# Kernel optimization log

Hardware: AMD Instinct MI355X
Metric: run time of the kernel (lower is better)

The kernel has to match this reference:

```python
import jax, jax.numpy as jnp
import numpy as np

B, C_IN, C_OUT, H, W_SP = 64, 256, 256, 32, 32
G = H * W_SP  # groups == H*W per module assert


def setup_inputs() -> dict:
    key = jax.random.key(0)
    k1, k2, k3 = jax.random.split(key, 3)
    x = jax.random.normal(k1, (B, C_IN, H, W_SP), dtype=jnp.float32)
    # grouped 1x1 conv == per-group linear: weight [G, C_out, C_in], bias [G, C_out]
    W = jax.random.normal(k2, (G, C_OUT, C_IN), dtype=jnp.float32) * (1.0 / np.sqrt(C_IN))
    b = jax.random.normal(k3, (G, C_OUT), dtype=jnp.float32) * 0.01
    return {"x": x, "W": W, "b": b}


def reference(x, W, b):
    Bn, Cin, Hn, Wn = x.shape
    Gn = Hn * Wn
    # permute(0,2,3,1).reshape(B,-1,1,1): channels-last flatten -> [B, G, C_in]
    xg = jnp.transpose(x, (0, 2, 3, 1)).reshape(Bn, Gn, Cin)
    # block-diagonal batched matmul per spatial position (group)
    out = jnp.einsum("bgi,goi->bgo", xg, W) + b  # [B, G, C_out]
    # view(B,H,W,C_out).permute(0,3,1,2)
    return jnp.transpose(out.reshape(Bn, Hn, Wn, -1), (0, 3, 1, 2))
```

## Files before the change

kernel.cpp:

```cpp
#include <hip/hip_runtime.h>
#include <hip/hip_bf16.h>

typedef __bf16 bf16x8 __attribute__((ext_vector_type(8)));
typedef float f32x4 __attribute__((ext_vector_type(4)));

#define GN    1024
#define BATCH 64
#define CIN   256
#define COUT  256
#define NG    4
#define A_ELEMS (BATCH * CIN)
#define WSLICE  8192

#define G_AS __attribute__((address_space(1)))
#define L_AS __attribute__((address_space(3)))

static __device__ __forceinline__ void gload16(const void* g, void* l) {
  __builtin_amdgcn_global_load_lds((const G_AS void*)g, (L_AS void*)l, 16, 0, 0);
}

static __device__ __forceinline__ ushort f2bf(float f) {
  __hip_bfloat16 h = __float2bfloat16(f);
  return *reinterpret_cast<ushort*>(&h);
}
static __device__ __forceinline__ float bf2f(ushort u) {
  uint v = (uint)u << 16;
  return *reinterpret_cast<float*>(&v);
}

__global__ __launch_bounds__(256) void k_transpose_convert(
    const float* __restrict__ x, ushort* __restrict__ xT)
{
  __shared__ float tile[64][65];
  const int g0 = blockIdx.x * 64;
  const int i0 = blockIdx.y * 64;
  const int b  = blockIdx.z;
  const int t  = threadIdx.x;
  const int a  = t & 15;
  const int r  = t >> 4;
  const int key = (b & 7) << 3;

  const float* xb = x + (size_t)b * CIN * GN;
#pragma unroll
  for (int p = 0; p < 4; ++p) {
    int ii = p * 16 + r;
    float4 v = *reinterpret_cast<const float4*>(
        &xb[(size_t)(i0 + ii) * GN + g0 + a * 4]);
    tile[ii][a * 4 + 0] = v.x;
    tile[ii][a * 4 + 1] = v.y;
    tile[ii][a * 4 + 2] = v.z;
    tile[ii][a * 4 + 3] = v.w;
  }
  __syncthreads();

  ushort* xTb = xT + (size_t)b * GN * CIN;
#pragma unroll
  for (int p = 0; p < 4; ++p) {
    int gg = p * 16 + r;
    ushort4 u;
    u.x = f2bf(tile[a * 4 + 0][gg]);
    u.y = f2bf(tile[a * 4 + 1][gg]);
    u.z = f2bf(tile[a * 4 + 2][gg]);
    u.w = f2bf(tile[a * 4 + 3][gg]);
    int isw = (i0 + a * 4) ^ key;
    *reinterpret_cast<ushort4*>(&xTb[(size_t)(g0 + gg) * CIN + isw]) = u;
  }
}

__global__ __launch_bounds__(256) void k_group_gemm(
    const ushort* __restrict__ xT, const float* __restrict__ W,
    const float* __restrict__ bias, float* __restrict__ out,
    ushort* __restrict__ outT, int use_ws)
{
  __shared__ __align__(16) unsigned char lds[2 * A_ELEMS * 2 + 4 * 2 * WSLICE];
  ushort* lA        = (ushort*)lds;
  unsigned char* lW = lds + 2 * A_ELEMS * 2;

  const int tid  = threadIdx.x;
  const int wave = tid >> 6;
  const int lane = tid & 63;
  const int g_base = blockIdx.x * NG;

  const int arow = lane & 15;
  const int colk = (lane >> 4) * 32;
  const int kq   = (lane >> 4) << 3;
  const int oc   = 64 * wave + arow;

  unsigned char* lWw = lW + wave * (2 * WSLICE);
  const int swz_src = ((lane & 7) ^ (lane >> 3)) << 4;
  const int wrow    = lane >> 3;

  auto stage_a = [&](int gg, int ab) {
    ushort* base = lA + ab * A_ELEMS;
#pragma unroll
    for (int j = 0; j < 8; ++j) {
      int b = 16 * wave + 2 * j + (lane >> 5);
      const ushort* gsrc = xT + ((size_t)b * GN + gg) * CIN + (lane & 31) * 8;
      gload16(gsrc, base + (16 * wave + 2 * j) * CIN);
    }
  };
  auto stage_w = [&](const float* wgp, int ks, int buf) {
    unsigned char* ldb = lWw + buf * WSLICE;
    const unsigned char* gb = (const unsigned char*)wgp + (size_t)ks * 128 + swz_src;
#pragma unroll
    for (int j = 0; j < 8; ++j) {
      gload16(gb + (size_t)(8 * j + wrow) * (CIN * 4), ldb + j * 1024);
    }
  };

  float bvv[NG][4];
#pragma unroll
  for (int gi = 0; gi < NG; ++gi)
#pragma unroll
    for (int n = 0; n < 4; ++n)
      bvv[gi][n] = bias[(g_base + gi) * COUT + oc + n * 16];
  __builtin_amdgcn_sched_barrier(0);

  stage_a(g_base, 0);
  __builtin_amdgcn_sched_barrier(0);
  {
    const float* wg0 = W + ((size_t)g_base * COUT + 64 * wave) * CIN;
    stage_w(wg0, 0, 0);
    __builtin_amdgcn_sched_barrier(0);
    stage_w(wg0, 1, 1);
    __builtin_amdgcn_sched_barrier(0);
  }
  asm volatile("s_waitcnt vmcnt(8)" ::: "memory");
  __builtin_amdgcn_sched_barrier(0);
  __builtin_amdgcn_s_barrier();

#pragma unroll
  for (int gi = 0; gi < NG; ++gi) {
    const int g = g_base + gi;
    const ushort* lAc = lA + (gi & 1) * A_ELEMS;
    const float* wgp  = W + ((size_t)g * COUT + 64 * wave) * CIN;

    f32x4 acc[4][4];
#pragma unroll
    for (int m = 0; m < 4; ++m)
#pragma unroll
      for (int n = 0; n < 4; ++n)
        acc[m][n] = {0.f, 0.f, 0.f, 0.f};

#pragma unroll
    for (int ks = 0; ks < 8; ++ks) {
      if (gi < NG - 1) {
        if (ks == 6) { asm volatile("s_waitcnt vmcnt(16)" ::: "memory"); }
        else         { asm volatile("s_waitcnt vmcnt(8)"  ::: "memory"); }
      } else {
        if (ks == 7) { asm volatile("s_waitcnt vmcnt(0)"  ::: "memory"); }
        else         { asm volatile("s_waitcnt vmcnt(8)"  ::: "memory"); }
      }
      __builtin_amdgcn_sched_barrier(0);

      unsigned char* wb = lWw + (ks & 1) * WSLICE;
      const int key = (arow & 7) << 4;

      float4 f[4][2];
#pragma unroll
      for (int n = 0; n < 4; ++n) {
        int r = n * 16 + arow;
        f[n][0] = *reinterpret_cast<const float4*>(wb + r * 128 + (colk ^ key));
        f[n][1] = *reinterpret_cast<const float4*>(wb + r * 128 + ((colk + 16) ^ key));
      }
      bf16x8 afr[4];
      const int i0 = ks * 32 + kq;
#pragma unroll
      for (int m = 0; m < 4; ++m) {
        int row = m * 16 + arow;
        afr[m] = *reinterpret_cast<const bf16x8*>(
            &lAc[row * CIN + (i0 ^ ((row & 7) << 3))]);
      }

      asm volatile("s_waitcnt lgkmcnt(0)" ::: "memory");
      __builtin_amdgcn_sched_barrier(0);
      if (ks < 6) stage_w(wgp, ks + 2, ks & 1);
      if (ks == 5 && gi < NG - 1) stage_a(g + 1, (gi & 1) ^ 1);
      __builtin_amdgcn_sched_barrier(0);

      bf16x8 bfr[4];
#pragma unroll
      for (int n = 0; n < 4; ++n) {
        bfr[n][0] = (__bf16)f[n][0].x; bfr[n][1] = (__bf16)f[n][0].y;
        bfr[n][2] = (__bf16)f[n][0].z; bfr[n][3] = (__bf16)f[n][0].w;
        bfr[n][4] = (__bf16)f[n][1].x; bfr[n][5] = (__bf16)f[n][1].y;
        bfr[n][6] = (__bf16)f[n][1].z; bfr[n][7] = (__bf16)f[n][1].w;
      }

      __builtin_amdgcn_s_setprio(1);
#pragma unroll
      for (int m = 0; m < 4; ++m)
#pragma unroll
        for (int n = 0; n < 4; ++n)
          acc[m][n] = __builtin_amdgcn_mfma_f32_16x16x32_bf16(
              afr[m], bfr[n], acc[m][n], 0, 0, 0);
      __builtin_amdgcn_s_setprio(0);
    }

    if (use_ws) {
#pragma unroll
      for (int m = 0; m < 4; ++m) {
#pragma unroll
        for (int n = 0; n < 4; ++n) {
          int o = oc + n * 16;
#pragma unroll
          for (int j = 0; j < 4; ++j) {
            int b = m * 16 + ((lane >> 4) << 2) + j;
            __hip_bfloat16 h = __float2bfloat16(acc[m][n][j] + bvv[gi][n]);
            outT[((size_t)b * GN + g) * COUT + o] = *reinterpret_cast<ushort*>(&h);
          }
        }
      }
    } else {
#pragma unroll
      for (int m = 0; m < 4; ++m) {
#pragma unroll
        for (int n = 0; n < 4; ++n) {
          int o = oc + n * 16;
#pragma unroll
          for (int j = 0; j < 4; ++j) {
            int b = m * 16 + ((lane >> 4) << 2) + j;
            out[((size_t)b * COUT + o) * GN + g] = acc[m][n][j] + bvv[gi][n];
          }
        }
      }
    }
    __builtin_amdgcn_sched_barrier(0);

    if (gi < NG - 1) {
      const float* wgn = W + ((size_t)(g + 1) * COUT + 64 * wave) * CIN;
      stage_w(wgn, 0, 0);
      __builtin_amdgcn_sched_barrier(0);
      stage_w(wgn, 1, 1);
      __builtin_amdgcn_sched_barrier(0);
      asm volatile("s_waitcnt vmcnt(8)" ::: "memory");
      __builtin_amdgcn_sched_barrier(0);
      __builtin_amdgcn_s_barrier();
    }
  }
}

__global__ __launch_bounds__(256) void k_transpose_out(
    const ushort* __restrict__ outT, float* __restrict__ out)
{
  __shared__ float tile[64][65];
  const int g0 = blockIdx.x * 64;
  const int o0 = blockIdx.y * 64;
  const int b  = blockIdx.z;
  const int t  = threadIdx.x;
  const int a  = t & 15;
  const int r  = t >> 4;

  const ushort* src = outT + (size_t)b * GN * COUT;
#pragma unroll
  for (int p = 0; p < 4; ++p) {
    int gl = p * 16 + r;
    ushort4 u = *reinterpret_cast<const ushort4*>(
        &src[(size_t)(g0 + gl) * COUT + o0 + a * 4]);
    tile[gl][a * 4 + 0] = bf2f(u.x);
    tile[gl][a * 4 + 1] = bf2f(u.y);
    tile[gl][a * 4 + 2] = bf2f(u.z);
    tile[gl][a * 4 + 3] = bf2f(u.w);
  }
  __syncthreads();

  float* dst = out + (size_t)b * COUT * GN;
#pragma unroll
  for (int p = 0; p < 4; ++p) {
    int ol = p * 16 + r;
    float4 v;
    v.x = tile[a * 4 + 0][ol];
    v.y = tile[a * 4 + 1][ol];
    v.z = tile[a * 4 + 2][ol];
    v.w = tile[a * 4 + 3][ol];
    *reinterpret_cast<float4*>(&dst[(size_t)(o0 + ol) * GN + g0 + a * 4]) = v;
  }
}

extern "C" void kernel_launch(void* const* d_in, const int* in_sizes, int n_in,
                              void* d_out, int out_size, void* d_ws, size_t ws_size,
                              hipStream_t stream) {
  const float* x  = (const float*)d_in[0];
  const float* W  = (const float*)d_in[1];
  const float* bs = (const float*)d_in[2];
  float* out      = (float*)d_out;

  const size_t xT_elems = (size_t)BATCH * GN * CIN;
  const size_t oT_elems = (size_t)BATCH * GN * COUT;
  const bool use_ws = ws_size >= (xT_elems + oT_elems) * sizeof(ushort);

  ushort* xT   = (ushort*)d_ws;
  ushort* outT = xT + xT_elems;

  dim3 grid1(GN / 64, CIN / 64, BATCH);
  k_transpose_convert<<<grid1, 256, 0, stream>>>(x, xT);
  k_group_gemm<<<GN / NG, 256, 0, stream>>>(xT, W, bs, out,
                                            use_ws ? outT : nullptr,
                                            use_ws ? 1 : 0);
  if (use_ws) {
    dim3 grid3(GN / 64, COUT / 64, BATCH);
    k_transpose_out<<<grid3, 256, 0, stream>>>(outT, out);
  }
}
```

Before: 111.2 us.

## Triple-buffer weight slices across groups and store bf16 output in batch-contiguous layout

Moves the per-wave weight staging from two buffers to a three-deep ring that continues across group boundaries, so the next group's first slices are prefetched during the current group instead of after its epilogue. The vmcnt waits come from a per-(group, k-step) table, and the A prefetch starts one step earlier. The intermediate bf16 output is changed to a [G][COUT][B] layout so each lane writes a packed ushort4. The output transpose kernel is rewritten to read that layout with 16-byte loads. This uses more LDS per block, which may lower occupancy, and the hand-tuned wait counts risk races if they are wrong.

```diff
diff --git a/kernel.cpp b/kernel.cpp
--- a/kernel.cpp
+++ b/kernel.cpp
@@ -11,12 +11,22 @@
 #define NG    4
 #define A_ELEMS (BATCH * CIN)
 #define WSLICE  8192
+#define NWBUF   3
 
 #define G_AS __attribute__((address_space(1)))
 #define L_AS __attribute__((address_space(3)))
 
 static __device__ __forceinline__ void gload16(const void* g, void* l) {
   __builtin_amdgcn_global_load_lds((const G_AS void*)g, (L_AS void*)l, 16, 0, 0);
+}
+
+static __device__ __forceinline__ void vmwait(int n) {
+  if (n == 0)       asm volatile("s_waitcnt vmcnt(0)"  ::: "memory");
+  else if (n == 8)  asm volatile("s_waitcnt vmcnt(8)"  ::: "memory");
+  else if (n == 16) asm volatile("s_waitcnt vmcnt(16)" ::: "memory");
+  else if (n == 24) asm volatile("s_waitcnt vmcnt(24)" ::: "memory");
+  else if (n == 32) asm volatile("s_waitcnt vmcnt(32)" ::: "memory");
+  else              asm volatile("s_waitcnt vmcnt(40)" ::: "memory");
 }
 
 static __device__ __forceinline__ ushort f2bf(float f) {
@@ -72,7 +82,7 @@
     const float* __restrict__ bias, float* __restrict__ out,
     ushort* __restrict__ outT, int use_ws)
 {
-  __shared__ __align__(16) unsigned char lds[2 * A_ELEMS * 2 + 4 * 2 * WSLICE];
+  __shared__ __align__(16) unsigned char lds[2 * A_ELEMS * 2 + 4 * NWBUF * WSLICE];
   ushort* lA        = (ushort*)lds;
   unsigned char* lW = lds + 2 * A_ELEMS * 2;
 
@@ -82,11 +92,12 @@
   const int g_base = blockIdx.x * NG;
 
   const int arow = lane & 15;
-  const int colk = (lane >> 4) * 32;
-  const int kq   = (lane >> 4) << 3;
+  const int q    = lane >> 4;
+  const int colk = q * 32;
+  const int kq   = q << 3;
   const int oc   = 64 * wave + arow;
 
-  unsigned char* lWw = lW + wave * (2 * WSLICE);
+  unsigned char* lWw = lW + wave * (NWBUF * WSLICE);
   const int swz_src = ((lane & 7) ^ (lane >> 3)) << 4;
   const int wrow    = lane >> 3;
 
@@ -99,14 +110,20 @@
       gload16(gsrc, base + (16 * wave + 2 * j) * CIN);
     }
   };
-  auto stage_w = [&](const float* wgp, int ks, int buf) {
+  auto stage_w = [&](int gg, int ksl, int buf) {
     unsigned char* ldb = lWw + buf * WSLICE;
-    const unsigned char* gb = (const unsigned char*)wgp + (size_t)ks * 128 + swz_src;
+    const unsigned char* gb = (const unsigned char*)(W + ((size_t)gg * COUT + 64 * wave) * CIN)
+                              + (size_t)ksl * 128 + swz_src;
 #pragma unroll
     for (int j = 0; j < 8; ++j) {
       gload16(gb + (size_t)(8 * j + wrow) * (CIN * 4), ldb + j * 1024);
     }
   };
+
+  const int NTAB[4][8] = {{16,16,16,16,16,16,24,24},
+                          {32,32,32,16,16,16,24,24},
+                          {32,32,32,16,16,16,24,24},
+                          {32,32,32,16,16,16, 8, 0}};
 
   float bvv[NG][4];
 #pragma unroll
@@ -118,14 +135,11 @@
 
   stage_a(g_base, 0);
   __builtin_amdgcn_sched_barrier(0);
-  {
-    const float* wg0 = W + ((size_t)g_base * COUT + 64 * wave) * CIN;
-    stage_w(wg0, 0, 0);
-    __builtin_amdgcn_sched_barrier(0);
-    stage_w(wg0, 1, 1);
-    __builtin_amdgcn_sched_barrier(0);
-  }
-  asm volatile("s_waitcnt vmcnt(8)" ::: "memory");
+  stage_w(g_base, 0, 0);
+  stage_w(g_base, 1, 1);
+  stage_w(g_base, 2, 2);
+  __builtin_amdgcn_sched_barrier(0);
+  vmwait(24);
   __builtin_amdgcn_sched_barrier(0);
   __builtin_amdgcn_s_barrier();
 
@@ -133,7 +147,6 @@
   for (int gi = 0; gi < NG; ++gi) {
     const int g = g_base + gi;
     const ushort* lAc = lA + (gi & 1) * A_ELEMS;
-    const float* wgp  = W + ((size_t)g * COUT + 64 * wave) * CIN;
 
     f32x4 acc[4][4];
 #pragma unroll
@@ -144,16 +157,11 @@
 
 #pragma unroll
     for (int ks = 0; ks < 8; ++ks) {
-      if (gi < NG - 1) {
-        if (ks == 6) { asm volatile("s_waitcnt vmcnt(16)" ::: "memory"); }
-        else         { asm volatile("s_waitcnt vmcnt(8)"  ::: "memory"); }
-      } else {
-        if (ks == 7) { asm volatile("s_waitcnt vmcnt(0)"  ::: "memory"); }
-        else         { asm volatile("s_waitcnt vmcnt(8)"  ::: "memory"); }
-      }
+      vmwait(NTAB[gi][ks]);
       __builtin_amdgcn_sched_barrier(0);
 
-      unsigned char* wb = lWw + (ks & 1) * WSLICE;
+      const int s = gi * 8 + ks;
+      unsigned char* wb = lWw + (s % 3) * WSLICE;
       const int key = (arow & 7) << 4;
 
       float4 f[4][2];
@@ -174,8 +182,11 @@
 
       asm volatile("s_waitcnt lgkmcnt(0)" ::: "memory");
       __builtin_amdgcn_sched_barrier(0);
-      if (ks < 6) stage_w(wgp, ks + 2, ks & 1);
-      if (ks == 5 && gi < NG - 1) stage_a(g + 1, (gi & 1) ^ 1);
+      if (s + 3 < NG * 8) {
+        const int s2 = s + 3;
+        stage_w(g_base + (s2 >> 3), s2 & 7, s2 % 3);
+      }
+      if (ks == 4 && gi < NG - 1) stage_a(g + 1, (gi & 1) ^ 1);
       __builtin_amdgcn_sched_barrier(0);
 
       bf16x8 bfr[4];
@@ -203,12 +214,13 @@
 #pragma unroll
         for (int n = 0; n < 4; ++n) {
           int o = oc + n * 16;
-#pragma unroll
-          for (int j = 0; j < 4; ++j) {
-            int b = m * 16 + ((lane >> 4) << 2) + j;
-            __hip_bfloat16 h = __float2bfloat16(acc[m][n][j] + bvv[gi][n]);
-            outT[((size_t)b * GN + g) * COUT + o] = *reinterpret_cast<ushort*>(&h);
-          }
+          ushort4 u;
+          u.x = f2bf(acc[m][n][0] + bvv[gi][n]);
+          u.y = f2bf(acc[m][n][1] + bvv[gi][n]);
+          u.z = f2bf(acc[m][n][2] + bvv[gi][n]);
+          u.w = f2bf(acc[m][n][3] + bvv[gi][n]);
+          *reinterpret_cast<ushort4*>(
+              &outT[((size_t)g * COUT + o) * BATCH + m * 16 + 4 * q]) = u;
         }
       }
     } else {
@@ -219,7 +231,7 @@
           int o = oc + n * 16;
 #pragma unroll
           for (int j = 0; j < 4; ++j) {
-            int b = m * 16 + ((lane >> 4) << 2) + j;
+            int b = m * 16 + 4 * q + j;
             out[((size_t)b * COUT + o) * GN + g] = acc[m][n][j] + bvv[gi][n];
           }
         }
@@ -228,12 +240,7 @@
     __builtin_amdgcn_sched_barrier(0);
 
     if (gi < NG - 1) {
-      const float* wgn = W + ((size_t)(g + 1) * COUT + 64 * wave) * CIN;
-      stage_w(wgn, 0, 0);
-      __builtin_amdgcn_sched_barrier(0);
-      stage_w(wgn, 1, 1);
-      __builtin_amdgcn_sched_barrier(0);
-      asm volatile("s_waitcnt vmcnt(8)" ::: "memory");
+      vmwait(40);
       __builtin_amdgcn_sched_barrier(0);
       __builtin_amdgcn_s_barrier();
     }
@@ -245,35 +252,36 @@
 {
   __shared__ float tile[64][65];
   const int g0 = blockIdx.x * 64;
-  const int o0 = blockIdx.y * 64;
-  const int b  = blockIdx.z;
+  const int o  = blockIdx.y;
   const int t  = threadIdx.x;
-  const int a  = t & 15;
-  const int r  = t >> 4;
-
-  const ushort* src = outT + (size_t)b * GN * COUT;
-#pragma unroll
-  for (int p = 0; p < 4; ++p) {
-    int gl = p * 16 + r;
-    ushort4 u = *reinterpret_cast<const ushort4*>(
-        &src[(size_t)(g0 + gl) * COUT + o0 + a * 4]);
-    tile[gl][a * 4 + 0] = bf2f(u.x);
-    tile[gl][a * 4 + 1] = bf2f(u.y);
-    tile[gl][a * 4 + 2] = bf2f(u.z);
-    tile[gl][a * 4 + 3] = bf2f(u.w);
+
+  {
+    const int a  = t & 7;
+#pragma unroll
+    for (int p = 0; p < 2; ++p) {
+      int gl = p * 32 + (t >> 3);
+      int4 raw = *reinterpret_cast<const int4*>(
+          &outT[((size_t)(g0 + gl) * COUT + o) * BATCH + a * 8]);
+      const ushort* us = reinterpret_cast<const ushort*>(&raw);
+#pragma unroll
+      for (int e = 0; e < 8; ++e) tile[gl][a * 8 + e] = bf2f(us[e]);
+    }
   }
   __syncthreads();
 
-  float* dst = out + (size_t)b * COUT * GN;
-#pragma unroll
-  for (int p = 0; p < 4; ++p) {
-    int ol = p * 16 + r;
-    float4 v;
-    v.x = tile[a * 4 + 0][ol];
-    v.y = tile[a * 4 + 1][ol];
-    v.z = tile[a * 4 + 2][ol];
-    v.w = tile[a * 4 + 3][ol];
-    *reinterpret_cast<float4*>(&dst[(size_t)(o0 + ol) * GN + g0 + a * 4]) = v;
+  {
+    const int a2 = t & 15;
+#pragma unroll
+    for (int p = 0; p < 4; ++p) {
+      int bl = p * 16 + (t >> 4);
+      float4 v;
+      v.x = tile[4 * a2 + 0][bl];
+      v.y = tile[4 * a2 + 1][bl];
+      v.z = tile[4 * a2 + 2][bl];
+      v.w = tile[4 * a2 + 3][bl];
+      *reinterpret_cast<float4*>(
+          &out[((size_t)bl * COUT + o) * GN + g0 + 4 * a2]) = v;
+    }
   }
 }
 
@@ -286,7 +294,7 @@
   float* out      = (float*)d_out;
 
   const size_t xT_elems = (size_t)BATCH * GN * CIN;
-  const size_t oT_elems = (size_t)BATCH * GN * COUT;
+  const size_t oT_elems = (size_t)GN * COUT * BATCH;
   const bool use_ws = ws_size >= (xT_elems + oT_elems) * sizeof(ushort);
 
   ushort* xT   = (ushort*)d_ws;
@@ -298,7 +306,7 @@
                                             use_ws ? outT : nullptr,
                                             use_ws ? 1 : 0);
   if (use_ws) {
-    dim3 grid3(GN / 64, COUT / 64, BATCH);
+    dim3 grid3(GN / 64, COUT);
     k_transpose_out<<<grid3, 256, 0, stream>>>(outT, out);
   }
 }
```

Result: slower. 113.8 us (+2.3%).

## Enlarge transpose tiles to 256x256 bf16 and stage A prefetch earlier

Applied to the files above, without the earlier changes.

Both transpose kernels now handle a 256x256 tile per block, held as bf16 in LDS. The input transpose converts to bf16 before storing into LDS, which halves LDS footprint and traffic, and the output transpose stores raw bf16 in LDS and converts on readout. The grids shrink to GN/256 x BATCH blocks, with 64 loop iterations per thread instead of 4. The GEMM now issues the next group's A staging one k-step earlier (ks==4 instead of 5) to hide its latency better. The risks are the large LDS use (~132KB per block), which limits occupancy, fewer blocks, and possible bank conflicts in the column-wise ushort reads.

```diff
diff --git a/kernel.cpp b/kernel.cpp
--- a/kernel.cpp
+++ b/kernel.cpp
@@ -31,39 +31,38 @@
 __global__ __launch_bounds__(256) void k_transpose_convert(
     const float* __restrict__ x, ushort* __restrict__ xT)
 {
-  __shared__ float tile[64][65];
-  const int g0 = blockIdx.x * 64;
-  const int i0 = blockIdx.y * 64;
-  const int b  = blockIdx.z;
-  const int t  = threadIdx.x;
-  const int a  = t & 15;
-  const int r  = t >> 4;
-  const int key = (b & 7) << 3;
+  __shared__ ushort tile[256][258];
+  const int g0   = blockIdx.x * 256;
+  const int b    = blockIdx.y;
+  const int t    = threadIdx.x;
+  const int lane = t & 63;
+  const int w    = t >> 6;
+  const int key  = (b & 7) << 3;
 
   const float* xb = x + (size_t)b * CIN * GN;
-#pragma unroll
-  for (int p = 0; p < 4; ++p) {
-    int ii = p * 16 + r;
-    float4 v = *reinterpret_cast<const float4*>(
-        &xb[(size_t)(i0 + ii) * GN + g0 + a * 4]);
-    tile[ii][a * 4 + 0] = v.x;
-    tile[ii][a * 4 + 1] = v.y;
-    tile[ii][a * 4 + 2] = v.z;
-    tile[ii][a * 4 + 3] = v.w;
+#pragma unroll 4
+  for (int r = 0; r < 64; ++r) {
+    int i = r * 4 + w;
+    float4 v = *reinterpret_cast<const float4*>(&xb[(size_t)i * GN + g0 + lane * 4]);
+    ushort2 p0, p1;
+    p0.x = f2bf(v.x); p0.y = f2bf(v.y);
+    p1.x = f2bf(v.z); p1.y = f2bf(v.w);
+    *reinterpret_cast<ushort2*>(&tile[i][lane * 4])     = p0;
+    *reinterpret_cast<ushort2*>(&tile[i][lane * 4 + 2]) = p1;
   }
   __syncthreads();
 
   ushort* xTb = xT + (size_t)b * GN * CIN;
-#pragma unroll
-  for (int p = 0; p < 4; ++p) {
-    int gg = p * 16 + r;
+#pragma unroll 4
+  for (int r = 0; r < 64; ++r) {
+    int g = r * 4 + w;
     ushort4 u;
-    u.x = f2bf(tile[a * 4 + 0][gg]);
-    u.y = f2bf(tile[a * 4 + 1][gg]);
-    u.z = f2bf(tile[a * 4 + 2][gg]);
-    u.w = f2bf(tile[a * 4 + 3][gg]);
-    int isw = (i0 + a * 4) ^ key;
-    *reinterpret_cast<ushort4*>(&xTb[(size_t)(g0 + gg) * CIN + isw]) = u;
+    u.x = tile[lane * 4 + 0][g];
+    u.y = tile[lane * 4 + 1][g];
+    u.z = tile[lane * 4 + 2][g];
+    u.w = tile[lane * 4 + 3][g];
+    int isw = (lane * 4) ^ key;
+    *reinterpret_cast<ushort4*>(&xTb[(size_t)(g0 + g) * CIN + isw]) = u;
   }
 }
 
@@ -175,7 +174,7 @@
       asm volatile("s_waitcnt lgkmcnt(0)" ::: "memory");
       __builtin_amdgcn_sched_barrier(0);
       if (ks < 6) stage_w(wgp, ks + 2, ks & 1);
-      if (ks == 5 && gi < NG - 1) stage_a(g + 1, (gi & 1) ^ 1);
+      if (ks == 4 && gi < NG - 1) stage_a(g + 1, (gi & 1) ^ 1);
       __builtin_amdgcn_sched_barrier(0);
 
       bf16x8 bfr[4];
@@ -243,37 +242,37 @@
 __global__ __launch_bounds__(256) void k_transpose_out(
     const ushort* __restrict__ outT, float* __restrict__ out)
 {
-  __shared__ float tile[64][65];
-  const int g0 = blockIdx.x * 64;
-  const int o0 = blockIdx.y * 64;
-  const int b  = blockIdx.z;
-  const int t  = threadIdx.x;
-  const int a  = t & 15;
-  const int r  = t >> 4;
+  __shared__ ushort tile[256][258];
+  const int g0   = blockIdx.x * 256;
+  const int b    = blockIdx.y;
+  const int t    = threadIdx.x;
+  const int lane = t & 63;
+  const int w    = t >> 6;
 
   const ushort* src = outT + (size_t)b * GN * COUT;
-#pragma unroll
-  for (int p = 0; p < 4; ++p) {
-    int gl = p * 16 + r;
-    ushort4 u = *reinterpret_cast<const ushort4*>(
-        &src[(size_t)(g0 + gl) * COUT + o0 + a * 4]);
-    tile[gl][a * 4 + 0] = bf2f(u.x);
-    tile[gl][a * 4 + 1] = bf2f(u.y);
-    tile[gl][a * 4 + 2] = bf2f(u.z);
-    tile[gl][a * 4 + 3] = bf2f(u.w);
+#pragma unroll 4
+  for (int r = 0; r < 32; ++r) {
+    int g = r * 8 + w * 2 + (lane >> 5);
+    int4 raw = *reinterpret_cast<const int4*>(
+        &src[(size_t)(g0 + g) * COUT + (lane & 31) * 8]);
+    const ushort2* ps = reinterpret_cast<const ushort2*>(&raw);
+    int col = (lane & 31) * 8;
+#pragma unroll
+    for (int k = 0; k < 4; ++k)
+      *reinterpret_cast<ushort2*>(&tile[g][col + 2 * k]) = ps[k];
   }
   __syncthreads();
 
   float* dst = out + (size_t)b * COUT * GN;
-#pragma unroll
-  for (int p = 0; p < 4; ++p) {
-    int ol = p * 16 + r;
+#pragma unroll 4
+  for (int r = 0; r < 64; ++r) {
+    int o = r * 4 + w;
     float4 v;
-    v.x = tile[a * 4 + 0][ol];
-    v.y = tile[a * 4 + 1][ol];
-    v.z = tile[a * 4 + 2][ol];
-    v.w = tile[a * 4 + 3][ol];
-    *reinterpret_cast<float4*>(&dst[(size_t)(o0 + ol) * GN + g0 + a * 4]) = v;
+    v.x = bf2f(tile[lane * 4 + 0][o]);
+    v.y = bf2f(tile[lane * 4 + 1][o]);
+    v.z = bf2f(tile[lane * 4 + 2][o]);
+    v.w = bf2f(tile[lane * 4 + 3][o]);
+    *reinterpret_cast<float4*>(&dst[(size_t)o * GN + g0 + lane * 4]) = v;
   }
 }
 
@@ -292,13 +291,13 @@
   ushort* xT   = (ushort*)d_ws;
   ushort* outT = xT + xT_elems;
 
-  dim3 grid1(GN / 64, CIN / 64, BATCH);
+  dim3 grid1(GN / 256, BATCH);
   k_transpose_convert<<<grid1, 256, 0, stream>>>(x, xT);
   k_group_gemm<<<GN / NG, 256, 0, stream>>>(xT, W, bs, out,
                                             use_ws ? outT : nullptr,
                                             use_ws ? 1 : 0);
   if (use_ws) {
-    dim3 grid3(GN / 64, COUT / 64, BATCH);
+    dim3 grid3(GN / 256, BATCH);
     k_transpose_out<<<grid3, 256, 0, stream>>>(outT, out);
   }
 }
```

Result: slower. 129.7 us (+16.7%).
